# Kernel tuning notes

Measured on AMD Instinct MI355X. Metric: run time of the kernel, lower is better.

## Reference

```python
import jax, jax.numpy as jnp
import numpy as np

TRANSFER_VOLUME = 0.1
KW = 1e-14  # water ion product
LN10 = float(np.log(10.0))


def binarize_weight(w):
    # clip to [-1,1], forward pass is sign(), gradient flows through the clip (STE)
    clipped = jnp.clip(w, -1.0, 1.0)
    rounded = jnp.sign(clipped)
    return clipped + jax.lax.stop_gradient(rounded - clipped)


def setup_inputs() -> dict:
    key = jax.random.key(0)
    kx, kw = jax.random.split(key)
    batch, n_in, n_out = 4096, 4096, 4096
    x = jax.random.uniform(kx, (batch, n_in), dtype=jnp.float32)
    w = jax.random.normal(kw, (n_in, n_out), dtype=jnp.float32)
    return {"x": x, "w": w}


def reference(x, w):
    binary_weights = binarize_weight(w)  # [n_in, n_out], values in {-1, 0, +1}
    input_sz = x.shape[1]
    input_h_conc = 10.0 ** (-x)                       # [B, n_in]
    input_oh_conc = KW / input_h_conc                  # [B, n_in]
    input_h_num_moles = input_h_conc * TRANSFER_VOLUME
    input_oh_num_moles = input_oh_conc * TRANSFER_VOLUME
    acid_moles_sum = input_h_num_moles @ binary_weights   # [B, n_out]
    base_moles_sum = input_oh_num_moles @ binary_weights  # [B, n_out]
    remaining_moles = acid_moles_sum - base_moles_sum
    acid_is_limiting = remaining_moles < 0
    remaining_moles_conc = jnp.abs(remaining_moles) / (input_sz * TRANSFER_VOLUME)
    resultant_h_conc = jnp.where(acid_is_limiting, KW / remaining_moles_conc, remaining_moles_conc)
    resultant_ph = -jnp.log(resultant_h_conc) / LN10
    return resultant_ph
```

## Files before the change

kernel.cpp:

```cpp
#include <hip/hip_runtime.h>
#include <math.h>

#define BATCH 4096
#define NIN   4096
#define NOUT  4096

#define BM 128
#define BN 128
#define BK 32
#define NSTAGE (NIN / BK)

typedef __attribute__((ext_vector_type(8))) short bf16x8;
typedef __attribute__((ext_vector_type(8))) unsigned short u16x8;
typedef __attribute__((ext_vector_type(4))) float f32x4;

__device__ __forceinline__ float2 compute_terms(float xv) {
    float h  = (float)exp10(-(double)xv);
    float oh = 1e-14f / h;
    return make_float2(h * 0.1f, oh * 0.1f);
}
__device__ __forceinline__ unsigned short bf16_rne(float v) {
    unsigned int b = __float_as_uint(v);
    return (unsigned short)((b + 0x7FFFu + ((b >> 16) & 1u)) >> 16);
}
__device__ __forceinline__ float signf_of(float wv) {
    return (wv > 0.f) ? 1.f : ((wv < 0.f) ? -1.f : 0.f);
}
__device__ __forceinline__ unsigned short signbf16_of(float wv) {
    return (wv > 0.f) ? 0x3F80u : ((wv < 0.f) ? 0xBF80u : 0u);
}

__global__ __launch_bounds__(256) void precompute_A(const float* __restrict__ x,
                                                    float* __restrict__ aaT,
                                                    unsigned short* __restrict__ ab) {
    __shared__ float tile[64][65];
    const int m0 = blockIdx.y * 64, k0 = blockIdx.x * 64;
    const int tid = threadIdx.x;
    #pragma unroll
    for (int it = 0; it < 4; ++it) {
        int idx = tid + it * 256;
        int row = idx >> 4, q = idx & 15;
        float4 xv = *(const float4*)(x + (size_t)(m0 + row) * NIN + k0 + q * 4);
        float2 t0 = compute_terms(xv.x), t1 = compute_terms(xv.y),
               t2 = compute_terms(xv.z), t3 = compute_terms(xv.w);
        *(ushort4*)(ab + (size_t)(m0 + row) * NIN + k0 + q * 4) =
            make_ushort4(bf16_rne(t0.y), bf16_rne(t1.y), bf16_rne(t2.y), bf16_rne(t3.y));
        tile[row][q * 4 + 0] = t0.x; tile[row][q * 4 + 1] = t1.x;
        tile[row][q * 4 + 2] = t2.x; tile[row][q * 4 + 3] = t3.x;
    }
    __syncthreads();
    #pragma unroll
    for (int it = 0; it < 4; ++it) {
        int idx = tid + it * 256;
        int krow = idx >> 4, q = idx & 15;
        float4 v = make_float4(tile[q * 4 + 0][krow], tile[q * 4 + 1][krow],
                               tile[q * 4 + 2][krow], tile[q * 4 + 3][krow]);
        *(float4*)(aaT + (size_t)(k0 + krow) * NIN + m0 + q * 4) = v;
    }
}

__global__ __launch_bounds__(256) void precompute_signT(const float* __restrict__ w,
                                                        unsigned short* __restrict__ sT) {
    __shared__ unsigned short tile[64][68];
    const int k0 = blockIdx.y * 64, n0 = blockIdx.x * 64;
    const int tid = threadIdx.x;
    #pragma unroll
    for (int it = 0; it < 4; ++it) {
        int idx = tid + it * 256;
        int krow = idx >> 4, q = idx & 15;
        float4 wv = *(const float4*)(w + (size_t)(k0 + krow) * NOUT + n0 + q * 4);
        *(ushort4*)&tile[krow][q * 4] =
            make_ushort4(signbf16_of(wv.x), signbf16_of(wv.y), signbf16_of(wv.z), signbf16_of(wv.w));
    }
    __syncthreads();
    #pragma unroll
    for (int it = 0; it < 2; ++it) {
        int idx = tid + it * 256;
        int n = idx >> 3, kc = idx & 7;
        u16x8 v;
        #pragma unroll
        for (int j = 0; j < 8; ++j) v[j] = tile[kc * 8 + j][n];
        *(u16x8*)(sT + (size_t)(n0 + n) * NIN + k0 + kc * 8) = v;
    }
}

#define LDS_AS0 0
#define LDS_AS1 16384
#define LDS_BS0 32768
#define LDS_BS1 49152
#define LDS_BT0 65536
#define LDS_BT1 73728

__global__ __launch_bounds__(256, 2) void acid_gemm_hyb(const float* __restrict__ AaT,
                                                        const unsigned short* __restrict__ Ab,
                                                        const unsigned short* __restrict__ SignT,
                                                        const float* __restrict__ W,
                                                        float* __restrict__ out) {
    __shared__ __align__(16) char smem[81920];
    float*          As0 = (float*)(smem + LDS_AS0);
    float*          As1 = (float*)(smem + LDS_AS1);
    float*          Bs0 = (float*)(smem + LDS_BS0);
    float*          Bs1 = (float*)(smem + LDS_BS1);
    unsigned short* Bt0 = (unsigned short*)(smem + LDS_BT0);
    unsigned short* Bt1 = (unsigned short*)(smem + LDS_BT1);
    float*          BoutH = (float*)smem;

    const int tid  = threadIdx.x;
    const int tx   = tid & 15;
    const int ty   = tid >> 4;
    const int lane = tid & 63;
    const int wv   = tid >> 6;
    const int g    = lane >> 4;
    const int r16  = lane & 15;
    const int bm0  = blockIdx.y * BM;
    const int bn0  = blockIdx.x * BN;

    float ma[8][8] = {}, ca[8][8] = {};
    f32x4 acc[2][8] = {};

    float4 areg[4];
    float4 wreg[2][2];
    u16x8  btreg[2];

    #define ISSUE_LOADS(s)                                                          \
        {                                                                           \
            const int k0_ = (s) * BK;                                               \
            _Pragma("unroll")                                                       \
            for (int r = 0; r < 4; ++r)                                             \
                areg[r] = *(const float4*)(AaT +                                    \
                    (size_t)(k0_ + (tid >> 3)) * NIN + bm0 + ((tid & 7) + 8 * r) * 4);\
            _Pragma("unroll")                                                       \
            for (int r = 0; r < 2; ++r)                                             \
                _Pragma("unroll")                                                   \
                for (int h = 0; h < 2; ++h)                                         \
                    wreg[r][h] = *(const float4*)(W +                               \
                        (size_t)(k0_ + (tid >> 4) + 16 * r) * NOUT + bn0 + h * 64 + (tid & 15) * 4);\
            _Pragma("unroll")                                                       \
            for (int j = 0; j < 2; ++j)                                             \
                btreg[j] = *(const u16x8*)(SignT +                                  \
                    (size_t)(bn0 + (tid >> 1)) * NIN + k0_ + ((tid & 1) * 2 + j) * 8);\
        }

    #define WRITE_LDS(asp, bsp, btp)                                                \
        {                                                                           \
            _Pragma("unroll")                                                       \
            for (int r = 0; r < 4; ++r)                                             \
                *(float4*)&(asp)[(tid >> 3) * 128 + ((tid & 7) + 8 * r) * 4] = areg[r];\
            _Pragma("unroll")                                                       \
            for (int r = 0; r < 2; ++r)                                             \
                _Pragma("unroll")                                                   \
                for (int h = 0; h < 2; ++h) {                                       \
                    float4 w_ = wreg[r][h];                                         \
                    *(float4*)&(bsp)[((tid >> 4) + 16 * r) * 128 + h * 64 + (tid & 15) * 4] = \
                        make_float4(signf_of(w_.x), signf_of(w_.y),                 \
                                    signf_of(w_.z), signf_of(w_.w));                \
                }                                                                   \
            {                                                                       \
                int row_ = tid >> 1;                                                \
                _Pragma("unroll")                                                   \
                for (int j = 0; j < 2; ++j) {                                       \
                    int c_ = (tid & 1) * 2 + j;                                     \
                    int cs_ = c_ ^ (row_ & 3);                                      \
                    *(u16x8*)&(btp)[row_ * 32 + cs_ * 8] = btreg[j];                \
                }                                                                   \
            }                                                                       \
        }

    #define STAGE(s, ASc, BSc, BTc, ASn, BSn, BTn)                                  \
        {                                                                           \
            const int k0c_ = (s) * BK;                                              \
            bf16x8 af0 = *(const bf16x8*)(Ab +                                      \
                (size_t)(bm0 + wv * 32 + r16) * NIN + k0c_ + g * 8);                \
            bf16x8 af1 = *(const bf16x8*)(Ab +                                      \
                (size_t)(bm0 + wv * 32 + 16 + r16) * NIN + k0c_ + g * 8);           \
            if ((s) + 1 < NSTAGE) WRITE_LDS(ASn, BSn, BTn);                         \
            if ((s) + 2 < NSTAGE) ISSUE_LOADS((s) + 2);                             \
            _Pragma("unroll")                                                       \
            for (int tc = 0; tc < 8; ++tc) {                                        \
                int row_ = tc * 16 + r16;                                           \
                int cs_ = g ^ (row_ & 3);                                           \
                bf16x8 bf = *(const bf16x8*)&(BTc)[row_ * 32 + cs_ * 8];            \
                acc[0][tc] = __builtin_amdgcn_mfma_f32_16x16x32_bf16(af0, bf, acc[0][tc], 0, 0, 0);\
                acc[1][tc] = __builtin_amdgcn_mfma_f32_16x16x32_bf16(af1, bf, acc[1][tc], 0, 0, 0);\
            }                                                                       \
            _Pragma("unroll 4")                                                     \
            for (int k = 0; k < BK; ++k) {                                          \
                const float4 pa = *(const float4*)&(ASc)[k * 128 + ty * 8];         \
                const float4 pb = *(const float4*)&(ASc)[k * 128 + ty * 8 + 4];     \
                const float4 s0 = *(const float4*)&(BSc)[k * 128 + tx * 4];         \
                const float4 s1 = *(const float4*)&(BSc)[k * 128 + 64 + tx * 4];    \
                const float av[8] = {pa.x, pa.y, pa.z, pa.w, pb.x, pb.y, pb.z, pb.w};\
                const float sn[8] = {s0.x, s0.y, s0.z, s0.w, s1.x, s1.y, s1.z, s1.w};\
                _Pragma("unroll")                                                   \
                for (int m = 0; m < 8; ++m)                                         \
                    _Pragma("unroll")                                               \
                    for (int n = 0; n < 8; ++n)                                     \
                        ca[m][n] = fmaf(av[m], sn[n], ca[m][n]);                    \
            }                                                                       \
            if ((((s) + 1) & 15) == 0) {                                            \
                _Pragma("unroll")                                                   \
                for (int m = 0; m < 8; ++m)                                         \
                    _Pragma("unroll")                                               \
                    for (int n = 0; n < 8; ++n) {                                   \
                        ma[m][n] += ca[m][n]; ca[m][n] = 0.f;                       \
                    }                                                               \
            }                                                                       \
            __syncthreads();                                                        \
        }

    ISSUE_LOADS(0);
    WRITE_LDS(As0, Bs0, Bt0);
    ISSUE_LOADS(1);
    __syncthreads();

    for (int s2 = 0; s2 < NSTAGE / 2; ++s2) {
        STAGE(2 * s2,     As0, Bs0, Bt0, As1, Bs1, Bt1);
        STAGE(2 * s2 + 1, As1, Bs1, Bt1, As0, Bs0, Bt0);
    }

    #pragma unroll
    for (int hh = 0; hh < 2; ++hh) {
        #pragma unroll
        for (int tr = 0; tr < 2; ++tr)
            #pragma unroll
            for (int tc = 0; tc < 4; ++tc)
                #pragma unroll
                for (int rr = 0; rr < 4; ++rr)
                    BoutH[(wv * 32 + tr * 16 + g * 4 + rr) * 68 + tc * 16 + r16] =
                        acc[tr][hh * 4 + tc][rr];
        __syncthreads();
        #pragma unroll
        for (int m = 0; m < 8; ++m) {
            int row = ty * 8 + m;
            const float4 bv = *(const float4*)&BoutH[row * 68 + tx * 4];
            const float bb[4] = {bv.x, bv.y, bv.z, bv.w};
            #pragma unroll
            for (int n = 0; n < 4; ++n) {
                float r    = ma[m][hh * 4 + n] - bb[n];
                float conc = fabsf(r) / 409.6f;
                float hc   = (r < 0.f) ? (1e-14f / conc) : conc;
                float ph   = (-logf(hc)) / 2.302585092994046f;
                out[(size_t)(bm0 + row) * NOUT + bn0 + hh * 64 + tx * 4 + n] = ph;
            }
        }
        __syncthreads();
    }
    #undef ISSUE_LOADS
    #undef WRITE_LDS
    #undef STAGE
}

__global__ __launch_bounds__(256, 2) void acid_gemm_fly(const float* __restrict__ X,
                                                        const float* __restrict__ W,
                                                        float* __restrict__ out) {
    __shared__ float2 Asf[BK][128 + 2];
    __shared__ float  Bsf[BK][64];
    const int tid = threadIdx.x;
    const int tx = tid & 15, ty = tid >> 4;
    const int bm0 = blockIdx.y * 128, bn0 = blockIdx.x * 64;
    float ma[8][4] = {}, mb[8][4] = {}, ca[8][4] = {}, cb[8][4] = {};
    for (int s = 0; s < NSTAGE; ++s) {
        const int k0 = s * BK;
        for (int idx = tid; idx < 128 * BK; idx += 256) {
            int m = idx >> 5, k = idx & 31;
            Asf[k][m] = compute_terms(X[(size_t)(bm0 + m) * NIN + k0 + k]);
        }
        for (int idx = tid; idx < BK * 64; idx += 256) {
            int k = idx >> 6, c = idx & 63;
            Bsf[k][c] = signf_of(W[(size_t)(k0 + k) * NOUT + bn0 + c]);
        }
        __syncthreads();
        #pragma unroll 4
        for (int k = 0; k < BK; ++k) {
            float2 av[8]; float sv[4];
            #pragma unroll
            for (int m = 0; m < 8; ++m) av[m] = Asf[k][ty * 8 + m];
            #pragma unroll
            for (int n = 0; n < 4; ++n) sv[n] = Bsf[k][tx * 4 + n];
            #pragma unroll
            for (int m = 0; m < 8; ++m)
                #pragma unroll
                for (int n = 0; n < 4; ++n) {
                    ca[m][n] = fmaf(av[m].x, sv[n], ca[m][n]);
                    cb[m][n] = fmaf(av[m].y, sv[n], cb[m][n]);
                }
        }
        if (((s + 1) & 15) == 0) {
            #pragma unroll
            for (int m = 0; m < 8; ++m)
                #pragma unroll
                for (int n = 0; n < 4; ++n) {
                    ma[m][n] += ca[m][n]; ca[m][n] = 0.f;
                    mb[m][n] += cb[m][n]; cb[m][n] = 0.f;
                }
        }
        __syncthreads();
    }
    #pragma unroll
    for (int m = 0; m < 8; ++m) {
        int row = bm0 + ty * 8 + m;
        #pragma unroll
        for (int n = 0; n < 4; ++n) {
            int col = bn0 + tx * 4 + n;
            float r = ma[m][n] - mb[m][n];
            float conc = fabsf(r) / 409.6f;
            float hc = (r < 0.f) ? (1e-14f / conc) : conc;
            out[(size_t)row * NOUT + col] = (-logf(hc)) / 2.302585092994046f;
        }
    }
}

extern "C" void kernel_launch(void* const* d_in, const int* in_sizes, int n_in,
                              void* d_out, int out_size, void* d_ws, size_t ws_size,
                              hipStream_t stream) {
    const float* x = (const float*)d_in[0];
    const float* w = (const float*)d_in[1];
    float* out = (float*)d_out;

    const size_t nElem  = (size_t)BATCH * NIN;
    const size_t needWs = nElem * 4 + nElem * 2 + nElem * 2;
    dim3 grid(NOUT / BN, BATCH / BM);

    if (ws_size >= needWs) {
        float*          aaT   = (float*)d_ws;
        unsigned short* ab    = (unsigned short*)((char*)d_ws + nElem * 4);
        unsigned short* signT = (unsigned short*)((char*)d_ws + nElem * 6);
        precompute_A    <<<dim3(64, 64), 256, 0, stream>>>(x, aaT, ab);
        precompute_signT<<<dim3(64, 64), 256, 0, stream>>>(w, signT);
        acid_gemm_hyb   <<<grid, dim3(256), 0, stream>>>(aaT, ab, signT, w, out);
    } else {
        acid_gemm_fly<<<dim3(NOUT / 64, BATCH / 128), dim3(256), 0, stream>>>(x, w, out);
    }
}
```

Before: 2.193 ms.

## Split hybrid kernel into separate MFMA base GEMM and VALU acid GEMM

Breaks the fused hybrid kernel into two kernels: an MFMA bf16 GEMM for the base (OH) term that writes an fp32 intermediate, and an fp32 VALU GEMM for the acid term that reads a precomputed float sign matrix through global_load_lds and subtracts the base result in its epilogue. The sign precompute now also emits a float sign matrix, so sign conversion and the mixed MFMA/VALU register pressure leave the main loop and the VALU kernel can target 3 blocks per CU. This costs extra workspace (16x elements), another full-size intermediate round trip through memory, and an extra launch. The fallback path calls precompute_signTF with aaT as its float-sign output, which makes precompute_A run a second time to restore it.

After: 2.237 ms. +2.0%, slower.

```diff
diff --git a/kernel.cpp b/kernel.cpp
--- a/kernel.cpp
+++ b/kernel.cpp
@@ -4,11 +4,7 @@
 #define BATCH 4096
 #define NIN   4096
 #define NOUT  4096
-
-#define BM 128
-#define BN 128
-#define BK 32
-#define NSTAGE (NIN / BK)
+#define NSTAGE32 128
 
 typedef __attribute__((ext_vector_type(8))) short bf16x8;
 typedef __attribute__((ext_vector_type(8))) unsigned short u16x8;
@@ -29,6 +25,11 @@
 __device__ __forceinline__ unsigned short signbf16_of(float wv) {
     return (wv > 0.f) ? 0x3F80u : ((wv < 0.f) ? 0xBF80u : 0u);
 }
+
+#define GLOAD16(g, l)                                                        \
+    __builtin_amdgcn_global_load_lds(                                        \
+        (const __attribute__((address_space(1))) void*)(g),                  \
+        (__attribute__((address_space(3))) void*)(l), 16, 0, 0)
 
 __global__ __launch_bounds__(256) void precompute_A(const float* __restrict__ x,
                                                     float* __restrict__ aaT,
@@ -59,8 +60,9 @@
     }
 }
 
-__global__ __launch_bounds__(256) void precompute_signT(const float* __restrict__ w,
-                                                        unsigned short* __restrict__ sT) {
+__global__ __launch_bounds__(256) void precompute_signTF(const float* __restrict__ w,
+                                                         unsigned short* __restrict__ sT,
+                                                         float* __restrict__ sF) {
     __shared__ unsigned short tile[64][68];
     const int k0 = blockIdx.y * 64, n0 = blockIdx.x * 64;
     const int tid = threadIdx.x;
@@ -71,6 +73,8 @@
         float4 wv = *(const float4*)(w + (size_t)(k0 + krow) * NOUT + n0 + q * 4);
         *(ushort4*)&tile[krow][q * 4] =
             make_ushort4(signbf16_of(wv.x), signbf16_of(wv.y), signbf16_of(wv.z), signbf16_of(wv.w));
+        *(float4*)(sF + (size_t)(k0 + krow) * NOUT + n0 + q * 4) =
+            make_float4(signf_of(wv.x), signf_of(wv.y), signf_of(wv.z), signf_of(wv.w));
     }
     __syncthreads();
     #pragma unroll
@@ -82,6 +86,149 @@
         for (int j = 0; j < 8; ++j) v[j] = tile[kc * 8 + j][n];
         *(u16x8*)(sT + (size_t)(n0 + n) * NIN + k0 + kc * 8) = v;
     }
+}
+
+__global__ __launch_bounds__(256) void base_gemm(const unsigned short* __restrict__ Ab,
+                                                 const unsigned short* __restrict__ SignT,
+                                                 float* __restrict__ BaseW) {
+    __shared__ float BoutH[128][68];
+    const int tid  = threadIdx.x;
+    const int lane = tid & 63;
+    const int wv   = tid >> 6;
+    const int g    = lane >> 4;
+    const int r16  = lane & 15;
+    const int tx   = tid & 15;
+    const int ty   = tid >> 4;
+    const int bm0  = blockIdx.y * 128;
+    const int bn0  = blockIdx.x * 128;
+
+    f32x4 acc[2][8] = {};
+
+    for (int s = 0; s < NSTAGE32; ++s) {
+        const int k0 = s * 32;
+        bf16x8 af0 = *(const bf16x8*)(Ab + (size_t)(bm0 + wv * 32 +      r16) * NIN + k0 + g * 8);
+        bf16x8 af1 = *(const bf16x8*)(Ab + (size_t)(bm0 + wv * 32 + 16 + r16) * NIN + k0 + g * 8);
+        #pragma unroll
+        for (int tc = 0; tc < 8; ++tc) {
+            bf16x8 bf = *(const bf16x8*)(SignT + (size_t)(bn0 + tc * 16 + r16) * NIN + k0 + g * 8);
+            acc[0][tc] = __builtin_amdgcn_mfma_f32_16x16x32_bf16(af0, bf, acc[0][tc], 0, 0, 0);
+            acc[1][tc] = __builtin_amdgcn_mfma_f32_16x16x32_bf16(af1, bf, acc[1][tc], 0, 0, 0);
+        }
+    }
+
+    #pragma unroll
+    for (int hh = 0; hh < 2; ++hh) {
+        #pragma unroll
+        for (int tr = 0; tr < 2; ++tr)
+            #pragma unroll
+            for (int tc = 0; tc < 4; ++tc)
+                #pragma unroll
+                for (int rr = 0; rr < 4; ++rr)
+                    BoutH[wv * 32 + tr * 16 + g * 4 + rr][tc * 16 + r16] = acc[tr][hh * 4 + tc][rr];
+        __syncthreads();
+        #pragma unroll
+        for (int m = 0; m < 8; ++m) {
+            int row = ty * 8 + m;
+            float4 bv = *(const float4*)&BoutH[row][tx * 4];
+            *(float4*)(BaseW + (size_t)(bm0 + row) * NOUT + bn0 + hh * 64 + tx * 4) = bv;
+        }
+        __syncthreads();
+    }
+}
+
+__global__ __launch_bounds__(256, 3) void acid_gemm_valu(const float* __restrict__ AaT,
+                                                         const float* __restrict__ SignF,
+                                                         const float* __restrict__ BaseW,
+                                                         float* __restrict__ out) {
+    __shared__ __align__(16) float As[2][16][128];
+    __shared__ __align__(16) float Bs[2][16][128];
+
+    const int tid = threadIdx.x;
+    const int tx  = tid & 15;
+    const int ty  = tid >> 4;
+    const int w   = tid >> 6;
+    const int l   = tid & 63;
+    const int bm0 = blockIdx.y * 128;
+    const int bn0 = blockIdx.x * 128;
+
+    const int lrow = (l >> 5);
+    const int lcol = (l & 31) * 4;
+
+    float ma[8][8] = {}, ca[8][8] = {};
+
+    #define AISSUE(s, b)                                                            \
+        {                                                                           \
+            const int k0_ = (s) * 16;                                               \
+            _Pragma("unroll")                                                       \
+            for (int j = 0; j < 2; ++j) {                                           \
+                const int kr_ = w * 4 + 2 * j;                                      \
+                GLOAD16(AaT   + (size_t)(k0_ + kr_ + lrow) * NIN + bm0 + lcol,      \
+                        &As[b][kr_][0]);                                            \
+                GLOAD16(SignF + (size_t)(k0_ + kr_ + lrow) * NIN + bn0 + lcol,      \
+                        &Bs[b][kr_][0]);                                            \
+            }                                                                       \
+        }
+
+    #define ACOMP(s, b)                                                             \
+        {                                                                           \
+            _Pragma("unroll 4")                                                     \
+            for (int k = 0; k < 16; ++k) {                                          \
+                const float4 pa = *(const float4*)&As[b][k][ty * 8];                \
+                const float4 pb = *(const float4*)&As[b][k][ty * 8 + 4];            \
+                const float4 s0 = *(const float4*)&Bs[b][k][tx * 4];                \
+                const float4 s1 = *(const float4*)&Bs[b][k][64 + tx * 4];           \
+                const float av[8] = {pa.x, pa.y, pa.z, pa.w, pb.x, pb.y, pb.z, pb.w};\
+                const float sn[8] = {s0.x, s0.y, s0.z, s0.w, s1.x, s1.y, s1.z, s1.w};\
+                _Pragma("unroll")                                                   \
+                for (int m = 0; m < 8; ++m)                                         \
+                    _Pragma("unroll")                                               \
+                    for (int n = 0; n < 8; ++n)                                     \
+                        ca[m][n] = fmaf(av[m], sn[n], ca[m][n]);                    \
+            }                                                                       \
+            if ((((s) + 1) & 31) == 0) {                                            \
+                _Pragma("unroll")                                                   \
+                for (int m = 0; m < 8; ++m)                                         \
+                    _Pragma("unroll")                                               \
+                    for (int n = 0; n < 8; ++n) {                                   \
+                        ma[m][n] += ca[m][n]; ca[m][n] = 0.f;                       \
+                    }                                                               \
+            }                                                                       \
+        }
+
+    AISSUE(0, 0);
+    __syncthreads();
+
+    for (int s2 = 0; s2 < 128; ++s2) {
+        const int s = 2 * s2;
+        AISSUE(s + 1, 1);
+        ACOMP(s, 0);
+        __syncthreads();
+        if (s + 2 < 256) AISSUE(s + 2, 0);
+        ACOMP(s + 1, 1);
+        __syncthreads();
+    }
+
+    #pragma unroll
+    for (int m = 0; m < 8; ++m) {
+        const int row = ty * 8 + m;
+        const float4 bv0 = *(const float4*)(BaseW + (size_t)(bm0 + row) * NOUT + bn0 + tx * 4);
+        const float4 bv1 = *(const float4*)(BaseW + (size_t)(bm0 + row) * NOUT + bn0 + 64 + tx * 4);
+        const float bb[8] = {bv0.x, bv0.y, bv0.z, bv0.w, bv1.x, bv1.y, bv1.z, bv1.w};
+        float ph[8];
+        #pragma unroll
+        for (int n = 0; n < 8; ++n) {
+            float r    = ma[m][n] - bb[n];
+            float conc = fabsf(r) / 409.6f;
+            float hc   = (r < 0.f) ? (1e-14f / conc) : conc;
+            ph[n]      = (-logf(hc)) / 2.302585092994046f;
+        }
+        *(float4*)(out + (size_t)(bm0 + row) * NOUT + bn0 + tx * 4) =
+            make_float4(ph[0], ph[1], ph[2], ph[3]);
+        *(float4*)(out + (size_t)(bm0 + row) * NOUT + bn0 + 64 + tx * 4) =
+            make_float4(ph[4], ph[5], ph[6], ph[7]);
+    }
+    #undef AISSUE
+    #undef ACOMP
 }
 
 #define LDS_AS0 0
@@ -112,19 +259,18 @@
     const int wv   = tid >> 6;
     const int g    = lane >> 4;
     const int r16  = lane & 15;
-    const int bm0  = blockIdx.y * BM;
-    const int bn0  = blockIdx.x * BN;
+    const int bm0  = blockIdx.y * 128;
+    const int bn0  = blockIdx.x * 128;
 
     float ma[8][8] = {}, ca[8][8] = {};
     f32x4 acc[2][8] = {};
-
     float4 areg[4];
     float4 wreg[2][2];
     u16x8  btreg[2];
 
     #define ISSUE_LOADS(s)                                                          \
         {                                                                           \
-            const int k0_ = (s) * BK;                                               \
+            const int k0_ = (s) * 32;                                               \
             _Pragma("unroll")                                                       \
             for (int r = 0; r < 4; ++r)                                             \
                 areg[r] = *(const float4*)(AaT +                                    \
@@ -168,13 +314,13 @@
 
     #define STAGE(s, ASc, BSc, BTc, ASn, BSn, BTn)                                  \
         {                                                                           \
-            const int k0c_ = (s) * BK;                                              \
+            const int k0c_ = (s) * 32;                                              \
             bf16x8 af0 = *(const bf16x8*)(Ab +                                      \
                 (size_t)(bm0 + wv * 32 + r16) * NIN + k0c_ + g * 8);                \
             bf16x8 af1 = *(const bf16x8*)(Ab +                                      \
                 (size_t)(bm0 + wv * 32 + 16 + r16) * NIN + k0c_ + g * 8);           \
-            if ((s) + 1 < NSTAGE) WRITE_LDS(ASn, BSn, BTn);                         \
-            if ((s) + 2 < NSTAGE) ISSUE_LOADS((s) + 2);                             \
+            if ((s) + 1 < NSTAGE32) WRITE_LDS(ASn, BSn, BTn);                       \
+            if ((s) + 2 < NSTAGE32) ISSUE_LOADS((s) + 2);                           \
             _Pragma("unroll")                                                       \
             for (int tc = 0; tc < 8; ++tc) {                                        \
                 int row_ = tc * 16 + r16;                                           \
@@ -184,7 +330,7 @@
                 acc[1][tc] = __builtin_amdgcn_mfma_f32_16x16x32_bf16(af1, bf, acc[1][tc], 0, 0, 0);\
             }                                                                       \
             _Pragma("unroll 4")                                                     \
-            for (int k = 0; k < BK; ++k) {                                          \
+            for (int k = 0; k < 32; ++k) {                                          \
                 const float4 pa = *(const float4*)&(ASc)[k * 128 + ty * 8];         \
                 const float4 pb = *(const float4*)&(ASc)[k * 128 + ty * 8 + 4];     \
                 const float4 s0 = *(const float4*)&(BSc)[k * 128 + tx * 4];         \
@@ -213,7 +359,7 @@
     ISSUE_LOADS(1);
     __syncthreads();
 
-    for (int s2 = 0; s2 < NSTAGE / 2; ++s2) {
+    for (int s2 = 0; s2 < NSTAGE32 / 2; ++s2) {
         STAGE(2 * s2,     As0, Bs0, Bt0, As1, Bs1, Bt1);
         STAGE(2 * s2 + 1, As1, Bs1, Bt1, As0, Bs0, Bt0);
     }
@@ -253,25 +399,25 @@
 __global__ __launch_bounds__(256, 2) void acid_gemm_fly(const float* __restrict__ X,
                                                         const float* __restrict__ W,
                                                         float* __restrict__ out) {
-    __shared__ float2 Asf[BK][128 + 2];
-    __shared__ float  Bsf[BK][64];
+    __shared__ float2 Asf[32][128 + 2];
+    __shared__ float  Bsf[32][64];
     const int tid = threadIdx.x;
     const int tx = tid & 15, ty = tid >> 4;
     const int bm0 = blockIdx.y * 128, bn0 = blockIdx.x * 64;
     float ma[8][4] = {}, mb[8][4] = {}, ca[8][4] = {}, cb[8][4] = {};
-    for (int s = 0; s < NSTAGE; ++s) {
-        const int k0 = s * BK;
-        for (int idx = tid; idx < 128 * BK; idx += 256) {
+    for (int s = 0; s < NSTAGE32; ++s) {
+        const int k0 = s * 32;
+        for (int idx = tid; idx < 128 * 32; idx += 256) {
             int m = idx >> 5, k = idx & 31;
             Asf[k][m] = compute_terms(X[(size_t)(bm0 + m) * NIN + k0 + k]);
         }
-        for (int idx = tid; idx < BK * 64; idx += 256) {
+        for (int idx = tid; idx < 32 * 64; idx += 256) {
             int k = idx >> 6, c = idx & 63;
             Bsf[k][c] = signf_of(W[(size_t)(k0 + k) * NOUT + bn0 + c]);
         }
         __syncthreads();
         #pragma unroll 4
-        for (int k = 0; k < BK; ++k) {
+        for (int k = 0; k < 32; ++k) {
             float2 av[8]; float sv[4];
             #pragma unroll
             for (int m = 0; m < 8; ++m) av[m] = Asf[k][ty * 8 + m];
@@ -317,17 +463,23 @@
     const float* w = (const float*)d_in[1];
     float* out = (float*)d_out;
 
-    const size_t nElem  = (size_t)BATCH * NIN;
-    const size_t needWs = nElem * 4 + nElem * 2 + nElem * 2;
-    dim3 grid(NOUT / BN, BATCH / BM);
-
-    if (ws_size >= needWs) {
-        float*          aaT   = (float*)d_ws;
-        unsigned short* ab    = (unsigned short*)((char*)d_ws + nElem * 4);
-        unsigned short* signT = (unsigned short*)((char*)d_ws + nElem * 6);
-        precompute_A    <<<dim3(64, 64), 256, 0, stream>>>(x, aaT, ab);
-        precompute_signT<<<dim3(64, 64), 256, 0, stream>>>(w, signT);
-        acid_gemm_hyb   <<<grid, dim3(256), 0, stream>>>(aaT, ab, signT, w, out);
+    const size_t nElem = (size_t)BATCH * NIN;
+    float*          aaT   = (float*)d_ws;
+    unsigned short* ab    = (unsigned short*)((char*)d_ws + nElem * 4);
+    unsigned short* signT = (unsigned short*)((char*)d_ws + nElem * 6);
+    float*          signF = (float*)((char*)d_ws + nElem * 8);
+    float*          baseW = (float*)((char*)d_ws + nElem * 12);
+
+    if (ws_size >= nElem * 16) {
+        precompute_A     <<<dim3(64, 64), 256, 0, stream>>>(x, aaT, ab);
+        precompute_signTF<<<dim3(64, 64), 256, 0, stream>>>(w, signT, signF);
+        base_gemm        <<<dim3(32, 32), 256, 0, stream>>>(ab, signT, baseW);
+        acid_gemm_valu   <<<dim3(32, 32), 256, 0, stream>>>(aaT, signF, baseW, out);
+    } else if (ws_size >= nElem * 8) {
+        precompute_A     <<<dim3(64, 64), 256, 0, stream>>>(x, aaT, ab);
+        precompute_signTF<<<dim3(64, 64), 256, 0, stream>>>(w, signT, aaT );
+        precompute_A     <<<dim3(64, 64), 256, 0, stream>>>(x, aaT, ab);
+        acid_gemm_hyb    <<<dim3(32, 32), 256, 0, stream>>>(aaT, ab, signT, w, out);
     } else {
         acid_gemm_fly<<<dim3(NOUT / 64, BATCH / 128), dim3(256), 0, stream>>>(x, w, out);
     }
```

## Merge precompute kernels, use direct global-to-LDS loads, split FP32 and MFMA phases

Applied to the files above, without the earlier changes.

Fuses the two precompute kernels into one launch that also writes a float sign matrix. The main GEMM now streams the FP32 acid operand and the precomputed float signs into LDS with global_load_lds, using smaller 16-deep double buffers so three blocks fit per CU. The bf16 MFMA base-term GEMM moves to a separate loop that reads operands straight from global memory instead of LDS. Output stores are vectorised. The aim is to cut register staging, sign conversion in the hot loop and LDS pressure. The cost is an extra 64MB workspace write and uncached global reads in the MFMA loop.

Result: faster. 2.001 ms (-8.8%).

```diff
diff --git a/kernel.cpp b/kernel.cpp
--- a/kernel.cpp
+++ b/kernel.cpp
@@ -4,11 +4,6 @@
 #define BATCH 4096
 #define NIN   4096
 #define NOUT  4096
-
-#define BM 128
-#define BN 128
-#define BK 32
-#define NSTAGE (NIN / BK)
 
 typedef __attribute__((ext_vector_type(8))) short bf16x8;
 typedef __attribute__((ext_vector_type(8))) unsigned short u16x8;
@@ -30,165 +25,114 @@
     return (wv > 0.f) ? 0x3F80u : ((wv < 0.f) ? 0xBF80u : 0u);
 }
 
-__global__ __launch_bounds__(256) void precompute_A(const float* __restrict__ x,
-                                                    float* __restrict__ aaT,
-                                                    unsigned short* __restrict__ ab) {
-    __shared__ float tile[64][65];
-    const int m0 = blockIdx.y * 64, k0 = blockIdx.x * 64;
+#define GLOAD16(g, l)                                                        \
+    __builtin_amdgcn_global_load_lds(                                        \
+        (const __attribute__((address_space(1))) void*)(g),                  \
+        (__attribute__((address_space(3))) void*)(l), 16, 0, 0)
+
+__global__ __launch_bounds__(256) void precompute_all(const float* __restrict__ x,
+                                                      const float* __restrict__ w,
+                                                      float* __restrict__ aaT,
+                                                      unsigned short* __restrict__ ab,
+                                                      unsigned short* __restrict__ sT,
+                                                      float* __restrict__ sF) {
     const int tid = threadIdx.x;
-    #pragma unroll
-    for (int it = 0; it < 4; ++it) {
-        int idx = tid + it * 256;
-        int row = idx >> 4, q = idx & 15;
-        float4 xv = *(const float4*)(x + (size_t)(m0 + row) * NIN + k0 + q * 4);
-        float2 t0 = compute_terms(xv.x), t1 = compute_terms(xv.y),
-               t2 = compute_terms(xv.z), t3 = compute_terms(xv.w);
-        *(ushort4*)(ab + (size_t)(m0 + row) * NIN + k0 + q * 4) =
-            make_ushort4(bf16_rne(t0.y), bf16_rne(t1.y), bf16_rne(t2.y), bf16_rne(t3.y));
-        tile[row][q * 4 + 0] = t0.x; tile[row][q * 4 + 1] = t1.x;
-        tile[row][q * 4 + 2] = t2.x; tile[row][q * 4 + 3] = t3.x;
-    }
-    __syncthreads();
-    #pragma unroll
-    for (int it = 0; it < 4; ++it) {
-        int idx = tid + it * 256;
-        int krow = idx >> 4, q = idx & 15;
-        float4 v = make_float4(tile[q * 4 + 0][krow], tile[q * 4 + 1][krow],
-                               tile[q * 4 + 2][krow], tile[q * 4 + 3][krow]);
-        *(float4*)(aaT + (size_t)(k0 + krow) * NIN + m0 + q * 4) = v;
-    }
-}
-
-__global__ __launch_bounds__(256) void precompute_signT(const float* __restrict__ w,
-                                                        unsigned short* __restrict__ sT) {
-    __shared__ unsigned short tile[64][68];
-    const int k0 = blockIdx.y * 64, n0 = blockIdx.x * 64;
+    if (blockIdx.y < 64) {
+        __shared__ float tile[64][65];
+        const int m0 = blockIdx.y * 64, k0 = blockIdx.x * 64;
+        #pragma unroll
+        for (int it = 0; it < 4; ++it) {
+            int idx = tid + it * 256;
+            int row = idx >> 4, q = idx & 15;
+            float4 xv = *(const float4*)(x + (size_t)(m0 + row) * NIN + k0 + q * 4);
+            float2 t0 = compute_terms(xv.x), t1 = compute_terms(xv.y),
+                   t2 = compute_terms(xv.z), t3 = compute_terms(xv.w);
+            *(ushort4*)(ab + (size_t)(m0 + row) * NIN + k0 + q * 4) =
+                make_ushort4(bf16_rne(t0.y), bf16_rne(t1.y), bf16_rne(t2.y), bf16_rne(t3.y));
+            tile[row][q * 4 + 0] = t0.x; tile[row][q * 4 + 1] = t1.x;
+            tile[row][q * 4 + 2] = t2.x; tile[row][q * 4 + 3] = t3.x;
+        }
+        __syncthreads();
+        #pragma unroll
+        for (int it = 0; it < 4; ++it) {
+            int idx = tid + it * 256;
+            int krow = idx >> 4, q = idx & 15;
+            float4 v = make_float4(tile[q * 4 + 0][krow], tile[q * 4 + 1][krow],
+                                   tile[q * 4 + 2][krow], tile[q * 4 + 3][krow]);
+            *(float4*)(aaT + (size_t)(k0 + krow) * NIN + m0 + q * 4) = v;
+        }
+    } else {
+        __shared__ unsigned short tileu[64][68];
+        const int k0 = (blockIdx.y - 64) * 64, n0 = blockIdx.x * 64;
+        #pragma unroll
+        for (int it = 0; it < 4; ++it) {
+            int idx = tid + it * 256;
+            int krow = idx >> 4, q = idx & 15;
+            float4 wv = *(const float4*)(w + (size_t)(k0 + krow) * NOUT + n0 + q * 4);
+            *(ushort4*)&tileu[krow][q * 4] =
+                make_ushort4(signbf16_of(wv.x), signbf16_of(wv.y), signbf16_of(wv.z), signbf16_of(wv.w));
+            *(float4*)(sF + (size_t)(k0 + krow) * NOUT + n0 + q * 4) =
+                make_float4(signf_of(wv.x), signf_of(wv.y), signf_of(wv.z), signf_of(wv.w));
+        }
+        __syncthreads();
+        #pragma unroll
+        for (int it = 0; it < 2; ++it) {
+            int idx = tid + it * 256;
+            int n = idx >> 3, kc = idx & 7;
+            u16x8 v;
+            #pragma unroll
+            for (int j = 0; j < 8; ++j) v[j] = tileu[kc * 8 + j][n];
+            *(u16x8*)(sT + (size_t)(n0 + n) * NIN + k0 + kc * 8) = v;
+        }
+    }
+}
+
+__global__ __launch_bounds__(256, 3) void acid_base_fused(const float* __restrict__ AaT,
+                                                          const float* __restrict__ SignF,
+                                                          const unsigned short* __restrict__ Ab,
+                                                          const unsigned short* __restrict__ SignT,
+                                                          float* __restrict__ out) {
+    __shared__ __align__(16) char smem[34816];
+    float (*As)[16][128] = (float (*)[16][128])smem;
+    float (*Bs)[16][128] = (float (*)[16][128])(smem + 16384);
+    float (*BoutH)[68]   = (float (*)[68])smem;
+
     const int tid = threadIdx.x;
-    #pragma unroll
-    for (int it = 0; it < 4; ++it) {
-        int idx = tid + it * 256;
-        int krow = idx >> 4, q = idx & 15;
-        float4 wv = *(const float4*)(w + (size_t)(k0 + krow) * NOUT + n0 + q * 4);
-        *(ushort4*)&tile[krow][q * 4] =
-            make_ushort4(signbf16_of(wv.x), signbf16_of(wv.y), signbf16_of(wv.z), signbf16_of(wv.w));
-    }
-    __syncthreads();
-    #pragma unroll
-    for (int it = 0; it < 2; ++it) {
-        int idx = tid + it * 256;
-        int n = idx >> 3, kc = idx & 7;
-        u16x8 v;
-        #pragma unroll
-        for (int j = 0; j < 8; ++j) v[j] = tile[kc * 8 + j][n];
-        *(u16x8*)(sT + (size_t)(n0 + n) * NIN + k0 + kc * 8) = v;
-    }
-}
-
-#define LDS_AS0 0
-#define LDS_AS1 16384
-#define LDS_BS0 32768
-#define LDS_BS1 49152
-#define LDS_BT0 65536
-#define LDS_BT1 73728
-
-__global__ __launch_bounds__(256, 2) void acid_gemm_hyb(const float* __restrict__ AaT,
-                                                        const unsigned short* __restrict__ Ab,
-                                                        const unsigned short* __restrict__ SignT,
-                                                        const float* __restrict__ W,
-                                                        float* __restrict__ out) {
-    __shared__ __align__(16) char smem[81920];
-    float*          As0 = (float*)(smem + LDS_AS0);
-    float*          As1 = (float*)(smem + LDS_AS1);
-    float*          Bs0 = (float*)(smem + LDS_BS0);
-    float*          Bs1 = (float*)(smem + LDS_BS1);
-    unsigned short* Bt0 = (unsigned short*)(smem + LDS_BT0);
-    unsigned short* Bt1 = (unsigned short*)(smem + LDS_BT1);
-    float*          BoutH = (float*)smem;
-
-    const int tid  = threadIdx.x;
-    const int tx   = tid & 15;
-    const int ty   = tid >> 4;
-    const int lane = tid & 63;
-    const int wv   = tid >> 6;
-    const int g    = lane >> 4;
-    const int r16  = lane & 15;
-    const int bm0  = blockIdx.y * BM;
-    const int bn0  = blockIdx.x * BN;
+    const int tx  = tid & 15;
+    const int ty  = tid >> 4;
+    const int w   = tid >> 6;
+    const int l   = tid & 63;
+    const int g   = l >> 4;
+    const int r16 = l & 15;
+    const int bm0 = blockIdx.y * 128;
+    const int bn0 = blockIdx.x * 128;
+
+    const int lrow = (l >> 5);
+    const int lcol = (l & 31) * 4;
 
     float ma[8][8] = {}, ca[8][8] = {};
-    f32x4 acc[2][8] = {};
-
-    float4 areg[4];
-    float4 wreg[2][2];
-    u16x8  btreg[2];
-
-    #define ISSUE_LOADS(s)                                                          \
+
+    #define AISSUE(s, b)                                                            \
         {                                                                           \
-            const int k0_ = (s) * BK;                                               \
+            const int k0_ = (s) * 16;                                               \
             _Pragma("unroll")                                                       \
-            for (int r = 0; r < 4; ++r)                                             \
-                areg[r] = *(const float4*)(AaT +                                    \
-                    (size_t)(k0_ + (tid >> 3)) * NIN + bm0 + ((tid & 7) + 8 * r) * 4);\
-            _Pragma("unroll")                                                       \
-            for (int r = 0; r < 2; ++r)                                             \
-                _Pragma("unroll")                                                   \
-                for (int h = 0; h < 2; ++h)                                         \
-                    wreg[r][h] = *(const float4*)(W +                               \
-                        (size_t)(k0_ + (tid >> 4) + 16 * r) * NOUT + bn0 + h * 64 + (tid & 15) * 4);\
-            _Pragma("unroll")                                                       \
-            for (int j = 0; j < 2; ++j)                                             \
-                btreg[j] = *(const u16x8*)(SignT +                                  \
-                    (size_t)(bn0 + (tid >> 1)) * NIN + k0_ + ((tid & 1) * 2 + j) * 8);\
-        }
-
-    #define WRITE_LDS(asp, bsp, btp)                                                \
+            for (int j = 0; j < 2; ++j) {                                           \
+                const int kr_ = w * 4 + 2 * j;                                      \
+                GLOAD16(AaT   + (size_t)(k0_ + kr_ + lrow) * NIN + bm0 + lcol,      \
+                        &As[b][kr_][0]);                                            \
+                GLOAD16(SignF + (size_t)(k0_ + kr_ + lrow) * NIN + bn0 + lcol,      \
+                        &Bs[b][kr_][0]);                                            \
+            }                                                                       \
+        }
+
+    #define ACOMP(s, b)                                                             \
         {                                                                           \
-            _Pragma("unroll")                                                       \
-            for (int r = 0; r < 4; ++r)                                             \
-                *(float4*)&(asp)[(tid >> 3) * 128 + ((tid & 7) + 8 * r) * 4] = areg[r];\
-            _Pragma("unroll")                                                       \
-            for (int r = 0; r < 2; ++r)                                             \
-                _Pragma("unroll")                                                   \
-                for (int h = 0; h < 2; ++h) {                                       \
-                    float4 w_ = wreg[r][h];                                         \
-                    *(float4*)&(bsp)[((tid >> 4) + 16 * r) * 128 + h * 64 + (tid & 15) * 4] = \
-                        make_float4(signf_of(w_.x), signf_of(w_.y),                 \
-                                    signf_of(w_.z), signf_of(w_.w));                \
-                }                                                                   \
-            {                                                                       \
-                int row_ = tid >> 1;                                                \
-                _Pragma("unroll")                                                   \
-                for (int j = 0; j < 2; ++j) {                                       \
-                    int c_ = (tid & 1) * 2 + j;                                     \
-                    int cs_ = c_ ^ (row_ & 3);                                      \
-                    *(u16x8*)&(btp)[row_ * 32 + cs_ * 8] = btreg[j];                \
-                }                                                                   \
-            }                                                                       \
-        }
-
-    #define STAGE(s, ASc, BSc, BTc, ASn, BSn, BTn)                                  \
-        {                                                                           \
-            const int k0c_ = (s) * BK;                                              \
-            bf16x8 af0 = *(const bf16x8*)(Ab +                                      \
-                (size_t)(bm0 + wv * 32 + r16) * NIN + k0c_ + g * 8);                \
-            bf16x8 af1 = *(const bf16x8*)(Ab +                                      \
-                (size_t)(bm0 + wv * 32 + 16 + r16) * NIN + k0c_ + g * 8);           \
-            if ((s) + 1 < NSTAGE) WRITE_LDS(ASn, BSn, BTn);                         \
-            if ((s) + 2 < NSTAGE) ISSUE_LOADS((s) + 2);                             \
-            _Pragma("unroll")                                                       \
-            for (int tc = 0; tc < 8; ++tc) {                                        \
-                int row_ = tc * 16 + r16;                                           \
-                int cs_ = g ^ (row_ & 3);                                           \
-                bf16x8 bf = *(const bf16x8*)&(BTc)[row_ * 32 + cs_ * 8];            \
-                acc[0][tc] = __builtin_amdgcn_mfma_f32_16x16x32_bf16(af0, bf, acc[0][tc], 0, 0, 0);\
-                acc[1][tc] = __builtin_amdgcn_mfma_f32_16x16x32_bf16(af1, bf, acc[1][tc], 0, 0, 0);\
-            }                                                                       \
             _Pragma("unroll 4")                                                     \
-            for (int k = 0; k < BK; ++k) {                                          \
-                const float4 pa = *(const float4*)&(ASc)[k * 128 + ty * 8];         \
-                const float4 pb = *(const float4*)&(ASc)[k * 128 + ty * 8 + 4];     \
-                const float4 s0 = *(const float4*)&(BSc)[k * 128 + tx * 4];         \
-                const float4 s1 = *(const float4*)&(BSc)[k * 128 + 64 + tx * 4];    \
+            for (int k = 0; k < 16; ++k) {                                          \
+                const float4 pa = *(const float4*)&As[b][k][ty * 8];                \
+                const float4 pb = *(const float4*)&As[b][k][ty * 8 + 4];            \
+                const float4 s0 = *(const float4*)&Bs[b][k][tx * 4];                \
+                const float4 s1 = *(const float4*)&Bs[b][k][64 + tx * 4];           \
                 const float av[8] = {pa.x, pa.y, pa.z, pa.w, pb.x, pb.y, pb.z, pb.w};\
                 const float sn[8] = {s0.x, s0.y, s0.z, s0.w, s1.x, s1.y, s1.z, s1.w};\
                 _Pragma("unroll")                                                   \
@@ -197,7 +141,7 @@
                     for (int n = 0; n < 8; ++n)                                     \
                         ca[m][n] = fmaf(av[m], sn[n], ca[m][n]);                    \
             }                                                                       \
-            if ((((s) + 1) & 15) == 0) {                                            \
+            if ((((s) + 1) & 31) == 0) {                                            \
                 _Pragma("unroll")                                                   \
                 for (int m = 0; m < 8; ++m)                                         \
                     _Pragma("unroll")                                               \
@@ -205,19 +149,40 @@
                         ma[m][n] += ca[m][n]; ca[m][n] = 0.f;                       \
                     }                                                               \
             }                                                                       \
-            __syncthreads();                                                        \
-        }
-
-    ISSUE_LOADS(0);
-    WRITE_LDS(As0, Bs0, Bt0);
-    ISSUE_LOADS(1);
+        }
+
+    AISSUE(0, 0);
     __syncthreads();
 
-    for (int s2 = 0; s2 < NSTAGE / 2; ++s2) {
-        STAGE(2 * s2,     As0, Bs0, Bt0, As1, Bs1, Bt1);
-        STAGE(2 * s2 + 1, As1, Bs1, Bt1, As0, Bs0, Bt0);
-    }
-
+    for (int s2 = 0; s2 < 128; ++s2) {
+        const int s = 2 * s2;
+        AISSUE(s + 1, 1);
+        ACOMP(s, 0);
+        __syncthreads();
+        if (s + 2 < 256) AISSUE(s + 2, 0);
+        ACOMP(s + 1, 1);
+        __syncthreads();
+    }
+
+    f32x4 acc[2][8] = {};
+    {
+        const unsigned short* a0 = Ab + (size_t)(bm0 + w * 32 + r16) * NIN + g * 8;
+        const unsigned short* a1 = Ab + (size_t)(bm0 + w * 32 + 16 + r16) * NIN + g * 8;
+        #pragma unroll 4
+        for (int s = 0; s < 128; ++s) {
+            const int k0 = s * 32;
+            bf16x8 af0 = *(const bf16x8*)(a0 + k0);
+            bf16x8 af1 = *(const bf16x8*)(a1 + k0);
+            #pragma unroll
+            for (int tc = 0; tc < 8; ++tc) {
+                bf16x8 bf = *(const bf16x8*)(SignT + (size_t)(bn0 + tc * 16 + r16) * NIN + k0 + g * 8);
+                acc[0][tc] = __builtin_amdgcn_mfma_f32_16x16x32_bf16(af0, bf, acc[0][tc], 0, 0, 0);
+                acc[1][tc] = __builtin_amdgcn_mfma_f32_16x16x32_bf16(af1, bf, acc[1][tc], 0, 0, 0);
+            }
+        }
+    }
+
+    __syncthreads();
     #pragma unroll
     for (int hh = 0; hh < 2; ++hh) {
         #pragma unroll
@@ -226,52 +191,52 @@
             for (int tc = 0; tc < 4; ++tc)
                 #pragma unroll
                 for (int rr = 0; rr < 4; ++rr)
-                    BoutH[(wv * 32 + tr * 16 + g * 4 + rr) * 68 + tc * 16 + r16] =
-                        acc[tr][hh * 4 + tc][rr];
+                    BoutH[w * 32 + tr * 16 + g * 4 + rr][tc * 16 + r16] = acc[tr][hh * 4 + tc][rr];
         __syncthreads();
         #pragma unroll
         for (int m = 0; m < 8; ++m) {
-            int row = ty * 8 + m;
-            const float4 bv = *(const float4*)&BoutH[row * 68 + tx * 4];
+            const int row = ty * 8 + m;
+            const float4 bv = *(const float4*)&BoutH[row][tx * 4];
             const float bb[4] = {bv.x, bv.y, bv.z, bv.w};
+            float ph[4];
             #pragma unroll
             for (int n = 0; n < 4; ++n) {
                 float r    = ma[m][hh * 4 + n] - bb[n];
                 float conc = fabsf(r) / 409.6f;
                 float hc   = (r < 0.f) ? (1e-14f / conc) : conc;
-                float ph   = (-logf(hc)) / 2.302585092994046f;
-                out[(size_t)(bm0 + row) * NOUT + bn0 + hh * 64 + tx * 4 + n] = ph;
+                ph[n]      = (-logf(hc)) / 2.302585092994046f;
             }
-        }
-        __syncthreads();
-    }
-    #undef ISSUE_LOADS
-    #undef WRITE_LDS
-    #undef STAGE
+            *(float4*)(out + (size_t)(bm0 + row) * NOUT + bn0 + hh * 64 + tx * 4) =
+                make_float4(ph[0], ph[1], ph[2], ph[3]);
+        }
+        __syncthreads();
+    }
+    #undef AISSUE
+    #undef ACOMP
 }
 
 __global__ __launch_bounds__(256, 2) void acid_gemm_fly(const float* __restrict__ X,
                                                         const float* __restrict__ W,
                                                         float* __restrict__ out) {
-    __shared__ float2 Asf[BK][128 + 2];
-    __shared__ float  Bsf[BK][64];
+    __shared__ float2 Asf[32][128 + 2];
+    __shared__ float  Bsf[32][64];
     const int tid = threadIdx.x;
     const int tx = tid & 15, ty = tid >> 4;
     const int bm0 = blockIdx.y * 128, bn0 = blockIdx.x * 64;
     float ma[8][4] = {}, mb[8][4] = {}, ca[8][4] = {}, cb[8][4] = {};
-    for (int s = 0; s < NSTAGE; ++s) {
-        const int k0 = s * BK;
-        for (int idx = tid; idx < 128 * BK; idx += 256) {
+    for (int s = 0; s < 128; ++s) {
+        const int k0 = s * 32;
+        for (int idx = tid; idx < 128 * 32; idx += 256) {
             int m = idx >> 5, k = idx & 31;
             Asf[k][m] = compute_terms(X[(size_t)(bm0 + m) * NIN + k0 + k]);
         }
-        for (int idx = tid; idx < BK * 64; idx += 256) {
+        for (int idx = tid; idx < 32 * 64; idx += 256) {
             int k = idx >> 6, c = idx & 63;
             Bsf[k][c] = signf_of(W[(size_t)(k0 + k) * NOUT + bn0 + c]);
         }
         __syncthreads();
         #pragma unroll 4
-        for (int k = 0; k < BK; ++k) {
+        for (int k = 0; k < 32; ++k) {
             float2 av[8]; float sv[4];
             #pragma unroll
             for (int m = 0; m < 8; ++m) av[m] = Asf[k][ty * 8 + m];
@@ -317,17 +282,15 @@
     const float* w = (const float*)d_in[1];
     float* out = (float*)d_out;
 
-    const size_t nElem  = (size_t)BATCH * NIN;
-    const size_t needWs = nElem * 4 + nElem * 2 + nElem * 2;
-    dim3 grid(NOUT / BN, BATCH / BM);
-
-    if (ws_size >= needWs) {
-        float*          aaT   = (float*)d_ws;
-        unsigned short* ab    = (unsigned short*)((char*)d_ws + nElem * 4);
-        unsigned short* signT = (unsigned short*)((char*)d_ws + nElem * 6);
-        precompute_A    <<<dim3(64, 64), 256, 0, stream>>>(x, aaT, ab);
-        precompute_signT<<<dim3(64, 64), 256, 0, stream>>>(w, signT);
-        acid_gemm_hyb   <<<grid, dim3(256), 0, stream>>>(aaT, ab, signT, w, out);
+    const size_t nElem = (size_t)BATCH * NIN;
+    float*          aaT   = (float*)d_ws;
+    unsigned short* ab    = (unsigned short*)((char*)d_ws + nElem * 4);
+    unsigned short* signT = (unsigned short*)((char*)d_ws + nElem * 6);
+    float*          signF = (float*)((char*)d_ws + nElem * 8);
+
+    if (ws_size >= nElem * 12) {
+        precompute_all <<<dim3(64, 128), 256, 0, stream>>>(x, w, aaT, ab, signT, signF);
+        acid_base_fused<<<dim3(32, 32), 256, 0, stream>>>(aaT, signF, ab, signT, out);
     } else {
         acid_gemm_fly<<<dim3(NOUT / 64, BATCH / 128), dim3(256), 0, stream>>>(x, w, out);
     }
```
